# Performance work log

Hardware: AMD Instinct MI355X
Metric: run time of the kernel (lower is better)

## Reference

```python
import jax, jax.numpy as jnp
import numpy as np

N_EMBD = 256
N_HEAD = 8
BATCH = 4
SEQ = 2048
NEG_BIAS = -1000000000.0


def setup_inputs() -> dict:
    key = jax.random.key(0)
    ks = jax.random.split(key, 5)
    scale = 1.0 / np.sqrt(N_EMBD)
    x = jax.random.normal(ks[0], (BATCH, SEQ, N_EMBD), dtype=jnp.float32)
    # torch Linear weight layout: (out_features, in_features)
    Wq = jax.random.normal(ks[1], (N_EMBD * N_HEAD, N_EMBD), dtype=jnp.float32) * scale
    Wk = jax.random.normal(ks[2], (N_EMBD * N_HEAD, N_EMBD), dtype=jnp.float32) * scale
    Wv = jax.random.normal(ks[3], (N_EMBD * N_HEAD, N_EMBD), dtype=jnp.float32) * scale
    Wo = jax.random.normal(ks[4], (N_EMBD, N_EMBD * N_HEAD), dtype=jnp.float32) * scale / np.sqrt(N_HEAD)
    return {"x": x, "Wq": Wq, "Wk": Wk, "Wv": Wv, "Wo": Wo}


def reference(x, Wq, Wk, Wv, Wo):
    B, L, E = x.shape
    H, D = N_HEAD, N_EMBD  # d_head == n_embd in this module
    # projections: x @ W.T, then split heads -> (B, H, L, D)
    def proj(W):
        y = jnp.einsum('ble,fe->blf', x, W)  # (B, L, H*D)
        return y.reshape(B, L, H, D).transpose(0, 2, 1, 3)
    q, k, v = proj(Wq), proj(Wk), proj(Wv)
    scores = jnp.einsum('bhld,bhmd->bhlm', q, k) * (E ** -0.5)
    # first (non-causal) softmax over full rows
    attn = jax.nn.softmax(scores, axis=-1)
    # causal mask replaces disallowed probs with large negative bias, then softmax again
    causal = jnp.tril(jnp.ones((L, L), dtype=bool))
    attn = jnp.where(causal[None, None], attn, jnp.asarray(NEG_BIAS, attn.dtype))
    attn = jax.nn.softmax(attn, axis=-1)
    out = jnp.einsum('bhlm,bhmd->bhld', attn, v)  # (B, H, L, D)
    out = out.transpose(0, 2, 1, 3).reshape(B, L, H * D)
    return jnp.einsum('blf,ef->ble', out, Wo)  # (B, L, E)
```

## Files before the change

kernel.cpp:

```cpp
#include <hip/hip_runtime.h>
#include <stdint.h>

typedef unsigned short ushort_t;
typedef __attribute__((ext_vector_type(8))) short bf16x8;
typedef __attribute__((ext_vector_type(4))) float f32x4;
typedef __attribute__((ext_vector_type(4))) unsigned short us4;

#define DEV __device__ __forceinline__

DEV ushort_t f2bf(float f) {
    unsigned int u = __float_as_uint(f);
    u += 0x7fffu + ((u >> 16) & 1u);
    return (ushort_t)(u >> 16);
}

DEV void async16(const ushort_t* g, ushort_t* l) {
    __builtin_amdgcn_global_load_lds(
        (const __attribute__((address_space(1))) void*)g,
        (__attribute__((address_space(3))) void*)l,
        16, 0, 0);
}

__global__ void convert_kernel(const float* __restrict__ x, const float* __restrict__ wq,
                               const float* __restrict__ wk, const float* __restrict__ wv,
                               const float* __restrict__ wo,
                               ushort_t* __restrict__ xb, ushort_t* __restrict__ wqb,
                               ushort_t* __restrict__ wkb, ushort_t* __restrict__ wvb,
                               ushort_t* __restrict__ wob)
{
    const int i = blockIdx.x * 256 + threadIdx.x;
    const float* src; ushort_t* dst; int off;
    if (i < 524288)      { src = x;  dst = xb;  off = i; }
    else if (i < 655360) { src = wq; dst = wqb; off = i - 524288; }
    else if (i < 786432) { src = wk; dst = wkb; off = i - 655360; }
    else if (i < 917504) { src = wv; dst = wvb; off = i - 786432; }
    else                 { src = wo; dst = wob; off = i - 917504; }
    const float4 v = ((const float4*)src)[off];
    us4 o;
    o[0] = f2bf(v.x); o[1] = f2bf(v.y); o[2] = f2bf(v.z); o[3] = f2bf(v.w);
    ((us4*)dst)[off] = o;
}

template <int MODE>
__global__ __launch_bounds__(256, 2) void gemm_bt_kernel(
    const ushort_t* __restrict__ A, const ushort_t* __restrict__ Bm,
    void* __restrict__ Cout, int M, int N, int K)
{
    __shared__ ushort_t At[128 * 64];
    __shared__ ushort_t Bt[128 * 64];

    const int tid  = threadIdx.x;
    const int wave = tid >> 6;
    const int lane = tid & 63;
    const int quad = lane >> 4;
    const int l15  = lane & 15;
    const int mhalf = wave >> 1;
    const int nhalf = wave & 1;
    const int m0 = blockIdx.x * 128;
    const int n0 = blockIdx.y * 128;

    f32x4 acc[4][4];
#pragma unroll
    for (int mf = 0; mf < 4; ++mf)
#pragma unroll
        for (int nf = 0; nf < 4; ++nf)
#pragma unroll
            for (int r = 0; r < 4; ++r) acc[mf][nf][r] = 0.f;

    const int crow = (lane & 7) ^ (lane >> 3);

    for (int k0 = 0; k0 < K; k0 += 64) {
        __syncthreads();
#pragma unroll
        for (int t = 0; t < 4; ++t) {
            const int row = wave * 32 + t * 8 + (lane >> 3);
            async16(A + (size_t)(m0 + row) * K + k0 + crow * 8,
                    At + (wave * 32 + t * 8) * 64 + lane * 8);
            async16(Bm + (size_t)(n0 + row) * K + k0 + crow * 8,
                    Bt + (wave * 32 + t * 8) * 64 + lane * 8);
        }
        __syncthreads();
#pragma unroll
        for (int ks = 0; ks < 2; ++ks) {
            bf16x8 af[4], bf[4];
#pragma unroll
            for (int mf = 0; mf < 4; ++mf) {
                const int ml = mhalf * 64 + mf * 16 + l15;
                const int c = (ks * 4 + quad) ^ (ml & 7);
                af[mf] = *(const bf16x8*)(At + ml * 64 + c * 8);
            }
#pragma unroll
            for (int nf = 0; nf < 4; ++nf) {
                const int nl = nhalf * 64 + nf * 16 + l15;
                const int c = (ks * 4 + quad) ^ (nl & 7);
                bf[nf] = *(const bf16x8*)(Bt + nl * 64 + c * 8);
            }
#pragma unroll
            for (int mf = 0; mf < 4; ++mf)
#pragma unroll
                for (int nf = 0; nf < 4; ++nf)
                    acc[mf][nf] = __builtin_amdgcn_mfma_f32_16x16x32_bf16(
                        af[mf], bf[nf], acc[mf][nf], 0, 0, 0);
        }
    }

    if (MODE == 1) {
#pragma unroll
        for (int mf = 0; mf < 4; ++mf)
#pragma unroll
            for (int nf = 0; nf < 4; ++nf) {
                const int row = m0 + mhalf * 64 + mf * 16 + quad * 4;
                const int col = n0 + nhalf * 64 + nf * 16 + l15;
                const int b_ = row >> 11, l_ = row & 2047;
                const int h_ = col >> 8, d_ = col & 255;
                us4 pk;
#pragma unroll
                for (int r = 0; r < 4; ++r) pk[r] = f2bf(acc[mf][nf][r]);
                *(us4*)((ushort_t*)Cout +
                        (((size_t)(b_ * 8 + h_) * 256 + d_) * 2048 + l_)) = pk;
            }
    } else {
#pragma unroll
        for (int mf = 0; mf < 4; ++mf)
#pragma unroll
            for (int nf = 0; nf < 4; ++nf)
#pragma unroll
                for (int r = 0; r < 4; ++r) {
                    const int row = m0 + mhalf * 64 + mf * 16 + quad * 4 + r;
                    const int col = n0 + nhalf * 64 + nf * 16 + l15;
                    if (MODE == 0)
                        ((ushort_t*)Cout)[(size_t)row * N + col] = f2bf(acc[mf][nf][r]);
                    else
                        ((float*)Cout)[(size_t)row * N + col] = acc[mf][nf][r];
                }
    }
}

__global__ __launch_bounds__(256, 4) void pass1_kernel(
    const ushort_t* __restrict__ q_ws, const ushort_t* __restrict__ k_ws,
    float* __restrict__ rz_ws)
{
    __shared__ ushort_t Kt[64 * 256];
    __shared__ float zred[2][64];

    const float SCALE = 0.0625f;
    const int tid  = threadIdx.x;
    const int wave = tid >> 6;
    const int lane = tid & 63;
    const int quad = lane >> 4;
    const int l15  = lane & 15;
    const int ihalf = wave >> 1;
    const int jhalf = wave & 1;

    const int g  = blockIdx.x;
    const int bh = ((g >> 8) << 3) | (g & 7);
    const int it = (g >> 3) & 31;
    const int b = bh >> 3, h = bh & 7;
    const int i0 = it * 64;

    const size_t qkbase = (size_t)b * 2048 * 2048 + (size_t)h * 256;

    bf16x8 qf[2][8];
#pragma unroll
    for (int ng = 0; ng < 2; ++ng) {
        const int i_l = ihalf * 32 + ng * 16 + l15;
        const ushort_t* qr = q_ws + qkbase + (size_t)(i0 + i_l) * 2048;
#pragma unroll
        for (int ks = 0; ks < 8; ++ks)
            qf[ng][ks] = *(const bf16x8*)(qr + ks * 32 + quad * 8);
    }

    float z[2] = {0.f, 0.f};

    for (int jt = 0; jt < 32; ++jt) {
        const int j0 = jt * 64;
        __syncthreads();
        {
            const ushort_t* kb = k_ws + qkbase + (size_t)j0 * 2048;
#pragma unroll
            for (int t = 0; t < 8; ++t) {
                const int row = wave * 16 + t * 2 + (lane >> 5);
                const int c = (lane & 31) ^ (row & 7);
                async16(kb + (size_t)row * 2048 + c * 8,
                        Kt + (wave * 16 + t * 2) * 256 + lane * 8);
            }
        }
        __syncthreads();

        f32x4 sacc[2][2];
#pragma unroll
        for (int a = 0; a < 2; ++a)
#pragma unroll
            for (int c = 0; c < 2; ++c)
#pragma unroll
                for (int r = 0; r < 4; ++r) sacc[a][c][r] = 0.f;

#pragma unroll
        for (int ks = 0; ks < 8; ++ks) {
            bf16x8 af[2];
#pragma unroll
            for (int mg = 0; mg < 2; ++mg) {
                const int j_l = jhalf * 32 + mg * 16 + l15;
                const int c = (ks * 4 + quad) ^ (j_l & 7);
                af[mg] = *(const bf16x8*)(Kt + j_l * 256 + c * 8);
            }
#pragma unroll
            for (int mg = 0; mg < 2; ++mg)
#pragma unroll
                for (int ng = 0; ng < 2; ++ng)
                    sacc[mg][ng] = __builtin_amdgcn_mfma_f32_16x16x32_bf16(
                        af[mg], qf[ng][ks], sacc[mg][ng], 0, 0, 0);
        }

#pragma unroll
        for (int ng = 0; ng < 2; ++ng)
#pragma unroll
            for (int mg = 0; mg < 2; ++mg)
#pragma unroll
                for (int r = 0; r < 4; ++r)
                    z[ng] += __expf(sacc[mg][ng][r] * SCALE);
    }

#pragma unroll
    for (int ng = 0; ng < 2; ++ng) {
        z[ng] += __shfl_xor(z[ng], 16);
        z[ng] += __shfl_xor(z[ng], 32);
    }
    __syncthreads();
    if (quad == 0) {
#pragma unroll
        for (int ng = 0; ng < 2; ++ng) {
            const int i_l = ihalf * 32 + ng * 16 + l15;
            zred[jhalf][i_l] = z[ng];
        }
    }
    __syncthreads();
    if (tid < 64)
        rz_ws[(size_t)bh * 2048 + i0 + tid] = 1.0f / (zred[0][tid] + zred[1][tid]);
}

__global__ __launch_bounds__(256, 2) void pass2_kernel(
    const ushort_t* __restrict__ q_ws, const ushort_t* __restrict__ k_ws,
    const ushort_t* __restrict__ vt_ws, const float* __restrict__ rz_ws,
    ushort_t* __restrict__ attn_out)
{
    __shared__ ushort_t smem[36864];
    ushort_t* Kt = smem;
    ushort_t* Vt = smem + 16384;
    ushort_t* Wt = smem + 32768;

    const float SCALE = 0.0625f;
    const int tid  = threadIdx.x;
    const int wave = tid >> 6;
    const int lane = tid & 63;
    const int quad = lane >> 4;
    const int l15  = lane & 15;
    const int ihalf = wave >> 1;
    const int jhalf = wave & 1;

    const int g  = blockIdx.x;
    const int bh = ((g >> 8) << 3) | (g & 7);
    const int it = 31 - ((g >> 3) & 31);
    const int b = bh >> 3, h = bh & 7;
    const int i0 = it * 64;

    const size_t qkbase = (size_t)b * 2048 * 2048 + (size_t)h * 256;

    bf16x8 qf[2][8];
#pragma unroll
    for (int ng = 0; ng < 2; ++ng) {
        const int i_l = ihalf * 32 + ng * 16 + l15;
        const ushort_t* qr = q_ws + qkbase + (size_t)(i0 + i_l) * 2048;
#pragma unroll
        for (int ks = 0; ks < 8; ++ks)
            qf[ng][ks] = *(const bf16x8*)(qr + ks * 32 + quad * 8);
    }

    float rzrow[2];
#pragma unroll
    for (int ng = 0; ng < 2; ++ng) {
        const int i_l = ihalf * 32 + ng * 16 + l15;
        rzrow[ng] = rz_ws[(size_t)bh * 2048 + i0 + i_l];
    }

    f32x4 oacc[2][8];
#pragma unroll
    for (int mg = 0; mg < 2; ++mg)
#pragma unroll
        for (int nf = 0; nf < 8; ++nf)
#pragma unroll
            for (int r = 0; r < 4; ++r) oacc[mg][nf][r] = 0.f;
    float den[2] = {0.f, 0.f};

    for (int jt = 0; jt <= it; ++jt) {
        const int j0 = jt * 64;
        const bool diag = (jt == it);
        __syncthreads();
        {
            const ushort_t* kb = k_ws + qkbase + (size_t)j0 * 2048;
#pragma unroll
            for (int t = 0; t < 8; ++t) {
                const int row = wave * 16 + t * 2 + (lane >> 5);
                const int c = (lane & 31) ^ (row & 7);
                async16(kb + (size_t)row * 2048 + c * 8,
                        Kt + (wave * 16 + t * 2) * 256 + lane * 8);
            }
            const ushort_t* vb = vt_ws + (size_t)bh * 256 * 2048 + j0;
#pragma unroll
            for (int t = 0; t < 8; ++t) {
                const int row = wave * 64 + t * 8 + (lane >> 3);
                const int c = (lane & 7) ^ (row & 7);
                async16(vb + (size_t)row * 2048 + c * 8,
                        Vt + (wave * 64 + t * 8) * 64 + lane * 8);
            }
        }
        __syncthreads();

        f32x4 sacc[2][2];
#pragma unroll
        for (int a = 0; a < 2; ++a)
#pragma unroll
            for (int c = 0; c < 2; ++c)
#pragma unroll
                for (int r = 0; r < 4; ++r) sacc[a][c][r] = 0.f;

#pragma unroll
        for (int ks = 0; ks < 8; ++ks) {
            bf16x8 af[2];
#pragma unroll
            for (int mg = 0; mg < 2; ++mg) {
                const int j_l = jhalf * 32 + mg * 16 + l15;
                const int c = (ks * 4 + quad) ^ (j_l & 7);
                af[mg] = *(const bf16x8*)(Kt + j_l * 256 + c * 8);
            }
#pragma unroll
            for (int mg = 0; mg < 2; ++mg)
#pragma unroll
                for (int ng = 0; ng < 2; ++ng)
                    sacc[mg][ng] = __builtin_amdgcn_mfma_f32_16x16x32_bf16(
                        af[mg], qf[ng][ks], sacc[mg][ng], 0, 0, 0);
        }

#pragma unroll
        for (int mg = 0; mg < 2; ++mg) {
#pragma unroll
            for (int ng = 0; ng < 2; ++ng) {
                const int i_l = ihalf * 32 + ng * 16 + l15;
                const int jb = jhalf * 32 + mg * 16 + quad * 4;
                us4 wp;
#pragma unroll
                for (int r = 0; r < 4; ++r) {
                    const float p = __expf(sacc[mg][ng][r] * SCALE) * rzrow[ng];
                    float w = __expf(p);
                    if (diag && (jb + r > i_l)) w = 0.f;
                    den[ng] += w;
                    wp[r] = f2bf(w);
                }
                const int c = (jb >> 3) ^ (i_l & 7);
                *(us4*)(Wt + i_l * 64 + c * 8 + (jb & 7)) = wp;
            }
        }
        __syncthreads();

#pragma unroll
        for (int ks = 0; ks < 2; ++ks) {
            bf16x8 aw[2];
#pragma unroll
            for (int mg = 0; mg < 2; ++mg) {
                const int i_l = ihalf * 32 + mg * 16 + l15;
                const int c = (ks * 4 + quad) ^ (i_l & 7);
                aw[mg] = *(const bf16x8*)(Wt + i_l * 64 + c * 8);
            }
#pragma unroll
            for (int nf = 0; nf < 8; ++nf) {
                const int d = jhalf * 128 + nf * 16 + l15;
                const int c = (ks * 4 + quad) ^ (d & 7);
                const bf16x8 bv = *(const bf16x8*)(Vt + d * 64 + c * 8);
                oacc[0][nf] = __builtin_amdgcn_mfma_f32_16x16x32_bf16(aw[0], bv, oacc[0][nf], 0, 0, 0);
                oacc[1][nf] = __builtin_amdgcn_mfma_f32_16x16x32_bf16(aw[1], bv, oacc[1][nf], 0, 0, 0);
            }
        }
    }

    __syncthreads();
    {
        float* dbuf = (float*)Kt;
#pragma unroll
        for (int ng = 0; ng < 2; ++ng) {
            const int i_l = ihalf * 32 + ng * 16 + l15;
            dbuf[(jhalf * 4 + quad) * 64 + i_l] = den[ng];
        }
    }
    __syncthreads();
    if (tid < 64) {
        const float* dbuf = (const float*)Kt;
        float s = 0.f;
#pragma unroll
        for (int p = 0; p < 8; ++p) s += dbuf[p * 64 + tid];
        ((float*)Kt)[512 + tid] = 1.0f / s;
    }
    __syncthreads();
    {
        const float* rden = (const float*)Kt + 512;
#pragma unroll
        for (int mg = 0; mg < 2; ++mg) {
#pragma unroll
            for (int r = 0; r < 4; ++r) {
                const int i_l = ihalf * 32 + mg * 16 + quad * 4 + r;
                const float rd = rden[i_l];
                ushort_t* orow = attn_out + qkbase + (size_t)(i0 + i_l) * 2048;
#pragma unroll
                for (int nf = 0; nf < 8; ++nf) {
                    const int d = jhalf * 128 + nf * 16 + l15;
                    orow[d] = f2bf(oacc[mg][nf][r] * rd);
                }
            }
        }
    }
}

extern "C" void kernel_launch(void* const* d_in, const int* in_sizes, int n_in,
                              void* d_out, int out_size, void* d_ws, size_t ws_size,
                              hipStream_t stream) {
    const float* x  = (const float*)d_in[0];
    const float* Wq = (const float*)d_in[1];
    const float* Wk = (const float*)d_in[2];
    const float* Wv = (const float*)d_in[3];
    const float* Wo = (const float*)d_in[4];

    char* ws = (char*)d_ws;
    ushort_t* xb    = (ushort_t*)(ws);
    ushort_t* wqb   = (ushort_t*)(ws + 4194304);
    ushort_t* wkb   = (ushort_t*)(ws + 5242880);
    ushort_t* wvb   = (ushort_t*)(ws + 6291456);
    ushort_t* wob   = (ushort_t*)(ws + 7340032);
    ushort_t* q_ws  = (ushort_t*)(ws + 8388608);
    ushort_t* k_ws  = (ushort_t*)(ws + 41943040);
    ushort_t* vt_ws = (ushort_t*)(ws + 75497472);
    ushort_t* ao_ws = (ushort_t*)(ws + 109051904);
    float*    rz_ws = (float*)   (ws + 142606336);

    convert_kernel<<<4096, 256, 0, stream>>>(x, Wq, Wk, Wv, Wo, xb, wqb, wkb, wvb, wob);

    dim3 gp(64, 16);
    gemm_bt_kernel<0><<<gp, 256, 0, stream>>>(xb, wqb, q_ws, 8192, 2048, 256);
    gemm_bt_kernel<0><<<gp, 256, 0, stream>>>(xb, wkb, k_ws, 8192, 2048, 256);
    gemm_bt_kernel<1><<<gp, 256, 0, stream>>>(xb, wvb, vt_ws, 8192, 2048, 256);

    pass1_kernel<<<1024, 256, 0, stream>>>(q_ws, k_ws, rz_ws);
    pass2_kernel<<<1024, 256, 0, stream>>>(q_ws, k_ws, vt_ws, rz_ws, ao_ws);

    gemm_bt_kernel<2><<<dim3(64, 2), 256, 0, stream>>>(ao_ws, wob, d_out, 8192, 256, 2048);
}
```

Measured before the change: 374.6 us.

## Materialize causal exp-scores in pass1 and skip QK recompute in pass2

Pass1 now writes bf16 exp(scaled scores) for the lower-triangular tiles to a workspace buffer. Pass2 reads these instead of recomputing Q·K^T, applies the row normalization and second exponential, and then runs only the P·V MMA. This removes half of the attention MMA work and the K loads from pass2, and allows higher occupancy. In exchange it adds roughly 70 MB of global writes and reads, introduces extra bf16 rounding of the probabilities, and falls back to the old kernel when the workspace is too small.

```diff
diff --git a/kernel.cpp b/kernel.cpp
--- a/kernel.cpp
+++ b/kernel.cpp
@@ -13,6 +13,8 @@
     u += 0x7fffu + ((u >> 16) & 1u);
     return (ushort_t)(u >> 16);
 }
+
+DEV float bf2f(ushort_t u) { return __uint_as_float(((unsigned int)u) << 16); }
 
 DEV void async16(const ushort_t* g, ushort_t* l) {
     __builtin_amdgcn_global_load_lds(
@@ -138,7 +140,7 @@
 
 __global__ __launch_bounds__(256, 4) void pass1_kernel(
     const ushort_t* __restrict__ q_ws, const ushort_t* __restrict__ k_ws,
-    float* __restrict__ rz_ws)
+    float* __restrict__ rz_ws, ushort_t* __restrict__ p_ws)
 {
     __shared__ ushort_t Kt[64 * 256];
     __shared__ float zred[2][64];
@@ -160,6 +162,10 @@
 
     const size_t qkbase = (size_t)b * 2048 * 2048 + (size_t)h * 256;
 
+    ushort_t* pbase = nullptr;
+    if (p_ws)
+        pbase = p_ws + ((size_t)bh * 528 + (size_t)it * (it + 1) / 2) * 4096;
+
     bf16x8 qf[2][8];
 #pragma unroll
     for (int ng = 0; ng < 2; ++ng) {
@@ -212,13 +218,28 @@
                         af[mg], qf[ng][ks], sacc[mg][ng], 0, 0, 0);
         }
 
+        const bool store = (pbase != nullptr) && (jt <= it);
 #pragma unroll
         for (int ng = 0; ng < 2; ++ng)
 #pragma unroll
-            for (int mg = 0; mg < 2; ++mg)
-#pragma unroll
-                for (int r = 0; r < 4; ++r)
-                    z[ng] += __expf(sacc[mg][ng][r] * SCALE);
+            for (int mg = 0; mg < 2; ++mg) {
+                if (store) {
+                    us4 pp;
+#pragma unroll
+                    for (int r = 0; r < 4; ++r) {
+                        const float e = __expf(sacc[mg][ng][r] * SCALE);
+                        z[ng] += e;
+                        pp[r] = f2bf(e);
+                    }
+                    const int i_l = ihalf * 32 + ng * 16 + l15;
+                    const int jb  = jhalf * 32 + mg * 16 + quad * 4;
+                    *(us4*)(pbase + (size_t)jt * 4096 + i_l * 64 + jb) = pp;
+                } else {
+#pragma unroll
+                    for (int r = 0; r < 4; ++r)
+                        z[ng] += __expf(sacc[mg][ng][r] * SCALE);
+                }
+            }
     }
 
 #pragma unroll
@@ -239,7 +260,151 @@
         rz_ws[(size_t)bh * 2048 + i0 + tid] = 1.0f / (zred[0][tid] + zred[1][tid]);
 }
 
-__global__ __launch_bounds__(256, 2) void pass2_kernel(
+__global__ __launch_bounds__(256, 4) void pass2_kernel(
+    const ushort_t* __restrict__ p_ws, const ushort_t* __restrict__ vt_ws,
+    const float* __restrict__ rz_ws, ushort_t* __restrict__ attn_out)
+{
+    __shared__ ushort_t smem[20480];
+    ushort_t* Vt = smem;
+    ushort_t* Wt = smem + 16384;
+
+    const int tid  = threadIdx.x;
+    const int wave = tid >> 6;
+    const int lane = tid & 63;
+    const int quad = lane >> 4;
+    const int l15  = lane & 15;
+    const int ihalf = wave >> 1;
+    const int jhalf = wave & 1;
+
+    const int g   = blockIdx.x;
+    const int rep = g >> 8;
+    const int x   = (g >> 3) & 31;
+    const int bh  = (rep << 3) | (g & 7);
+    int it;
+    if (rep == 0)      it = x;
+    else if (rep == 1) it = 31 - x;
+    else if (rep == 2) it = (x + 16) & 31;
+    else               it = (15 - x) & 31;
+    const int b = bh >> 3, h = bh & 7;
+    const int i0 = it * 64;
+
+    const size_t obase = (size_t)b * 2048 * 2048 + (size_t)h * 256;
+    const ushort_t* ptile =
+        p_ws + ((size_t)bh * 528 + (size_t)it * (it + 1) / 2) * 4096;
+
+    float rzrow[2];
+#pragma unroll
+    for (int ng = 0; ng < 2; ++ng) {
+        const int i_l = ihalf * 32 + ng * 16 + l15;
+        rzrow[ng] = rz_ws[(size_t)bh * 2048 + i0 + i_l];
+    }
+
+    f32x4 oacc[2][8];
+#pragma unroll
+    for (int mg = 0; mg < 2; ++mg)
+#pragma unroll
+        for (int nf = 0; nf < 8; ++nf)
+#pragma unroll
+            for (int r = 0; r < 4; ++r) oacc[mg][nf][r] = 0.f;
+    float den[2] = {0.f, 0.f};
+
+    for (int jt = 0; jt <= it; ++jt) {
+        const int j0 = jt * 64;
+        const bool diag = (jt == it);
+        __syncthreads();
+        {
+            const ushort_t* vb = vt_ws + (size_t)bh * 256 * 2048 + j0;
+#pragma unroll
+            for (int t = 0; t < 8; ++t) {
+                const int row = wave * 64 + t * 8 + (lane >> 3);
+                const int c = (lane & 7) ^ (row & 7);
+                async16(vb + (size_t)row * 2048 + c * 8,
+                        Vt + (wave * 64 + t * 8) * 64 + lane * 8);
+            }
+        }
+        {
+            const ushort_t* pb = ptile + (size_t)jt * 4096;
+#pragma unroll
+            for (int mg = 0; mg < 2; ++mg) {
+#pragma unroll
+                for (int ng = 0; ng < 2; ++ng) {
+                    const int i_l = ihalf * 32 + ng * 16 + l15;
+                    const int jb  = jhalf * 32 + mg * 16 + quad * 4;
+                    const us4 pp = *(const us4*)(pb + i_l * 64 + jb);
+                    us4 wp;
+#pragma unroll
+                    for (int r = 0; r < 4; ++r) {
+                        const float p = bf2f(pp[r]) * rzrow[ng];
+                        float w = __expf(p);
+                        if (diag && (jb + r > i_l)) w = 0.f;
+                        den[ng] += w;
+                        wp[r] = f2bf(w);
+                    }
+                    const int c = (jb >> 3) ^ (i_l & 7);
+                    *(us4*)(Wt + i_l * 64 + c * 8 + (jb & 7)) = wp;
+                }
+            }
+        }
+        __syncthreads();
+
+#pragma unroll
+        for (int ks = 0; ks < 2; ++ks) {
+            bf16x8 aw[2];
+#pragma unroll
+            for (int mg = 0; mg < 2; ++mg) {
+                const int i_l = ihalf * 32 + mg * 16 + l15;
+                const int c = (ks * 4 + quad) ^ (i_l & 7);
+                aw[mg] = *(const bf16x8*)(Wt + i_l * 64 + c * 8);
+            }
+#pragma unroll
+            for (int nf = 0; nf < 8; ++nf) {
+                const int d = jhalf * 128 + nf * 16 + l15;
+                const int c = (ks * 4 + quad) ^ (d & 7);
+                const bf16x8 bv = *(const bf16x8*)(Vt + d * 64 + c * 8);
+                oacc[0][nf] = __builtin_amdgcn_mfma_f32_16x16x32_bf16(aw[0], bv, oacc[0][nf], 0, 0, 0);
+                oacc[1][nf] = __builtin_amdgcn_mfma_f32_16x16x32_bf16(aw[1], bv, oacc[1][nf], 0, 0, 0);
+            }
+        }
+    }
+
+    __syncthreads();
+    {
+        float* dbuf = (float*)smem;
+#pragma unroll
+        for (int ng = 0; ng < 2; ++ng) {
+            const int i_l = ihalf * 32 + ng * 16 + l15;
+            dbuf[(jhalf * 4 + quad) * 64 + i_l] = den[ng];
+        }
+    }
+    __syncthreads();
+    if (tid < 64) {
+        const float* dbuf = (const float*)smem;
+        float s = 0.f;
+#pragma unroll
+        for (int p = 0; p < 8; ++p) s += dbuf[p * 64 + tid];
+        ((float*)smem)[512 + tid] = 1.0f / s;
+    }
+    __syncthreads();
+    {
+        const float* rden = (const float*)smem + 512;
+#pragma unroll
+        for (int mg = 0; mg < 2; ++mg) {
+#pragma unroll
+            for (int r = 0; r < 4; ++r) {
+                const int i_l = ihalf * 32 + mg * 16 + quad * 4 + r;
+                const float rd = rden[i_l];
+                ushort_t* orow = attn_out + obase + (size_t)(i0 + i_l) * 2048;
+#pragma unroll
+                for (int nf = 0; nf < 8; ++nf) {
+                    const int d = jhalf * 128 + nf * 16 + l15;
+                    orow[d] = f2bf(oacc[mg][nf][r] * rd);
+                }
+            }
+        }
+    }
+}
+
+__global__ __launch_bounds__(256, 2) void pass2_fb_kernel(
     const ushort_t* __restrict__ q_ws, const ushort_t* __restrict__ k_ws,
     const ushort_t* __restrict__ vt_ws, const float* __restrict__ rz_ws,
     ushort_t* __restrict__ attn_out)
@@ -440,6 +605,11 @@
     ushort_t* ao_ws = (ushort_t*)(ws + 109051904);
     float*    rz_ws = (float*)   (ws + 142606336);
 
+    const size_t P_OFF   = 142868480ull;
+    const size_t P_BYTES = 32ull * 528 * 4096 * 2;
+    const bool use_p = ws_size >= P_OFF + P_BYTES;
+    ushort_t* p_ws = use_p ? (ushort_t*)(ws + P_OFF) : (ushort_t*)0;
+
     convert_kernel<<<4096, 256, 0, stream>>>(x, Wq, Wk, Wv, Wo, xb, wqb, wkb, wvb, wob);
 
     dim3 gp(64, 16);
@@ -447,8 +617,11 @@
     gemm_bt_kernel<0><<<gp, 256, 0, stream>>>(xb, wkb, k_ws, 8192, 2048, 256);
     gemm_bt_kernel<1><<<gp, 256, 0, stream>>>(xb, wvb, vt_ws, 8192, 2048, 256);
 
-    pass1_kernel<<<1024, 256, 0, stream>>>(q_ws, k_ws, rz_ws);
-    pass2_kernel<<<1024, 256, 0, stream>>>(q_ws, k_ws, vt_ws, rz_ws, ao_ws);
+    pass1_kernel<<<1024, 256, 0, stream>>>(q_ws, k_ws, rz_ws, p_ws);
+    if (use_p)
+        pass2_kernel<<<1024, 256, 0, stream>>>(p_ws, vt_ws, rz_ws, ao_ws);
+    else
+        pass2_fb_kernel<<<1024, 256, 0, stream>>>(q_ws, k_ws, vt_ws, rz_ws, ao_ws);
 
     gemm_bt_kernel<2><<<dim3(64, 2), 256, 0, stream>>>(ao_ws, wob, d_out, 8192, 256, 2048);
 }
```

After: 380.0 us. Within noise of the previous version (+1.4%).

## Merge QKV projection launches and stage attention output through LDS for coalesced stores

Applied to the files above, without the earlier changes.

Replaces the three separate projection GEMM launches with one launch using a z grid dimension that picks the weight and output. Separately, pass2 now writes its normalized output tile into a swizzled LDS buffer and then stores it to global memory with 16-byte vector writes, replacing scattered 2-byte stores. The goal is fewer launches and better-coalesced global writes, at the cost of an extra barrier and LDS traffic in pass2. The output GEMM is split into its own float-output kernel with the same body.

```diff
diff --git a/kernel.cpp b/kernel.cpp
--- a/kernel.cpp
+++ b/kernel.cpp
@@ -41,13 +41,18 @@
     ((us4*)dst)[off] = o;
 }
 
-template <int MODE>
-__global__ __launch_bounds__(256, 2) void gemm_bt_kernel(
-    const ushort_t* __restrict__ A, const ushort_t* __restrict__ Bm,
-    void* __restrict__ Cout, int M, int N, int K)
+__global__ __launch_bounds__(256, 2) void qkv_gemm_kernel(
+    const ushort_t* __restrict__ A, const ushort_t* __restrict__ wq,
+    const ushort_t* __restrict__ wk, const ushort_t* __restrict__ wv,
+    ushort_t* __restrict__ q_out, ushort_t* __restrict__ k_out,
+    ushort_t* __restrict__ vt_out)
 {
     __shared__ ushort_t At[128 * 64];
     __shared__ ushort_t Bt[128 * 64];
+
+    const int K = 256, N = 2048;
+    const int z = blockIdx.z;
+    const ushort_t* Bm = (z == 0) ? wq : (z == 1) ? wk : wv;
 
     const int tid  = threadIdx.x;
     const int wave = tid >> 6;
@@ -104,7 +109,7 @@
         }
     }
 
-    if (MODE == 1) {
+    if (z == 2) {
 #pragma unroll
         for (int mf = 0; mf < 4; ++mf)
 #pragma unroll
@@ -116,10 +121,10 @@
                 us4 pk;
 #pragma unroll
                 for (int r = 0; r < 4; ++r) pk[r] = f2bf(acc[mf][nf][r]);
-                *(us4*)((ushort_t*)Cout +
-                        (((size_t)(b_ * 8 + h_) * 256 + d_) * 2048 + l_)) = pk;
+                *(us4*)(vt_out + (((size_t)(b_ * 8 + h_) * 256 + d_) * 2048 + l_)) = pk;
             }
     } else {
+        ushort_t* Cout = z ? k_out : q_out;
 #pragma unroll
         for (int mf = 0; mf < 4; ++mf)
 #pragma unroll
@@ -128,12 +133,83 @@
                 for (int r = 0; r < 4; ++r) {
                     const int row = m0 + mhalf * 64 + mf * 16 + quad * 4 + r;
                     const int col = n0 + nhalf * 64 + nf * 16 + l15;
-                    if (MODE == 0)
-                        ((ushort_t*)Cout)[(size_t)row * N + col] = f2bf(acc[mf][nf][r]);
-                    else
-                        ((float*)Cout)[(size_t)row * N + col] = acc[mf][nf][r];
+                    Cout[(size_t)row * N + col] = f2bf(acc[mf][nf][r]);
                 }
     }
+}
+
+__global__ __launch_bounds__(256, 2) void out_gemm_kernel(
+    const ushort_t* __restrict__ A, const ushort_t* __restrict__ Bm,
+    float* __restrict__ Cout, int M, int N, int K)
+{
+    __shared__ ushort_t At[128 * 64];
+    __shared__ ushort_t Bt[128 * 64];
+
+    const int tid  = threadIdx.x;
+    const int wave = tid >> 6;
+    const int lane = tid & 63;
+    const int quad = lane >> 4;
+    const int l15  = lane & 15;
+    const int mhalf = wave >> 1;
+    const int nhalf = wave & 1;
+    const int m0 = blockIdx.x * 128;
+    const int n0 = blockIdx.y * 128;
+
+    f32x4 acc[4][4];
+#pragma unroll
+    for (int mf = 0; mf < 4; ++mf)
+#pragma unroll
+        for (int nf = 0; nf < 4; ++nf)
+#pragma unroll
+            for (int r = 0; r < 4; ++r) acc[mf][nf][r] = 0.f;
+
+    const int crow = (lane & 7) ^ (lane >> 3);
+
+    for (int k0 = 0; k0 < K; k0 += 64) {
+        __syncthreads();
+#pragma unroll
+        for (int t = 0; t < 4; ++t) {
+            const int row = wave * 32 + t * 8 + (lane >> 3);
+            async16(A + (size_t)(m0 + row) * K + k0 + crow * 8,
+                    At + (wave * 32 + t * 8) * 64 + lane * 8);
+            async16(Bm + (size_t)(n0 + row) * K + k0 + crow * 8,
+                    Bt + (wave * 32 + t * 8) * 64 + lane * 8);
+        }
+        __syncthreads();
+#pragma unroll
+        for (int ks = 0; ks < 2; ++ks) {
+            bf16x8 af[4], bf[4];
+#pragma unroll
+            for (int mf = 0; mf < 4; ++mf) {
+                const int ml = mhalf * 64 + mf * 16 + l15;
+                const int c = (ks * 4 + quad) ^ (ml & 7);
+                af[mf] = *(const bf16x8*)(At + ml * 64 + c * 8);
+            }
+#pragma unroll
+            for (int nf = 0; nf < 4; ++nf) {
+                const int nl = nhalf * 64 + nf * 16 + l15;
+                const int c = (ks * 4 + quad) ^ (nl & 7);
+                bf[nf] = *(const bf16x8*)(Bt + nl * 64 + c * 8);
+            }
+#pragma unroll
+            for (int mf = 0; mf < 4; ++mf)
+#pragma unroll
+                for (int nf = 0; nf < 4; ++nf)
+                    acc[mf][nf] = __builtin_amdgcn_mfma_f32_16x16x32_bf16(
+                        af[mf], bf[nf], acc[mf][nf], 0, 0, 0);
+        }
+    }
+
+#pragma unroll
+    for (int mf = 0; mf < 4; ++mf)
+#pragma unroll
+        for (int nf = 0; nf < 4; ++nf)
+#pragma unroll
+            for (int r = 0; r < 4; ++r) {
+                const int row = m0 + mhalf * 64 + mf * 16 + quad * 4 + r;
+                const int col = n0 + nhalf * 64 + nf * 16 + l15;
+                Cout[(size_t)row * N + col] = acc[mf][nf][r];
+            }
 }
 
 __global__ __launch_bounds__(256, 4) void pass1_kernel(
@@ -406,15 +482,27 @@
         for (int mg = 0; mg < 2; ++mg) {
 #pragma unroll
             for (int r = 0; r < 4; ++r) {
-                const int i_l = ihalf * 32 + mg * 16 + quad * 4 + r;
-                const float rd = rden[i_l];
-                ushort_t* orow = attn_out + qkbase + (size_t)(i0 + i_l) * 2048;
+                const int row = ihalf * 32 + mg * 16 + quad * 4 + r;
+                const float rd = rden[row];
 #pragma unroll
                 for (int nf = 0; nf < 8; ++nf) {
                     const int d = jhalf * 128 + nf * 16 + l15;
-                    orow[d] = f2bf(oacc[mg][nf][r] * rd);
+                    const int xu = (d >> 3) ^ (row & 31);
+                    Vt[row * 256 + xu * 8 + (d & 7)] = f2bf(oacc[mg][nf][r] * rd);
                 }
             }
+        }
+    }
+    __syncthreads();
+    {
+        const int row = tid >> 2;
+        const int q4  = tid & 3;
+        const ushort_t* Vr = Vt + row * 256;
+        ushort_t* orow = attn_out + qkbase + (size_t)(i0 + row) * 2048 + q4 * 64;
+#pragma unroll
+        for (int k = 0; k < 8; ++k) {
+            const int xu = (q4 * 8 + k) ^ (row & 31);
+            *(bf16x8*)(orow + k * 8) = *(const bf16x8*)(Vr + xu * 8);
         }
     }
 }
@@ -442,13 +530,11 @@
 
     convert_kernel<<<4096, 256, 0, stream>>>(x, Wq, Wk, Wv, Wo, xb, wqb, wkb, wvb, wob);
 
-    dim3 gp(64, 16);
-    gemm_bt_kernel<0><<<gp, 256, 0, stream>>>(xb, wqb, q_ws, 8192, 2048, 256);
-    gemm_bt_kernel<0><<<gp, 256, 0, stream>>>(xb, wkb, k_ws, 8192, 2048, 256);
-    gemm_bt_kernel<1><<<gp, 256, 0, stream>>>(xb, wvb, vt_ws, 8192, 2048, 256);
+    qkv_gemm_kernel<<<dim3(64, 16, 3), 256, 0, stream>>>(
+        xb, wqb, wkb, wvb, q_ws, k_ws, vt_ws);
 
     pass1_kernel<<<1024, 256, 0, stream>>>(q_ws, k_ws, rz_ws);
     pass2_kernel<<<1024, 256, 0, stream>>>(q_ws, k_ws, vt_ws, rz_ws, ao_ws);
 
-    gemm_bt_kernel<2><<<dim3(64, 2), 256, 0, stream>>>(ao_ws, wob, d_out, 8192, 256, 2048);
-}
+    out_gemm_kernel<<<dim3(64, 2), 256, 0, stream>>>(ao_ws, wob, (float*)d_out, 8192, 256, 2048);
+}
```

New measurement: 356.8 us. -4.7%, faster.
